# Kernel optimization log

Hardware: AMD Instinct MI355X
Metric: run time of the kernel (lower is better)

The kernel has to match this reference:

```python
import jax, jax.numpy as jnp
import numpy as np

N_USERS = 200000
N_ITEMS = 100000
N_NODES = N_USERS + N_ITEMS
N_EDGES = 1500000
EMBED_DIM = 64
BERT_DIM = 384
N_LAYERS = 3


def setup_inputs() -> dict:
    key = jax.random.key(0)
    ks = jax.random.split(key, 13)
    return {
        "user_emb": jax.random.normal(ks[0], (N_USERS, EMBED_DIM), jnp.float32) * 0.1,
        "item_emb": jax.random.normal(ks[1], (N_ITEMS, EMBED_DIM), jnp.float32) * 0.1,
        "gender_emb": jax.random.normal(ks[2], (3, EMBED_DIM), jnp.float32) * 0.1,
        "age_emb": jax.random.normal(ks[3], (8, EMBED_DIM), jnp.float32) * 0.1,
        "cat_emb": jax.random.normal(ks[4], (11, EMBED_DIM), jnp.float32) * 0.1,
        "bert_proj_w": jax.random.normal(ks[5], (EMBED_DIM, BERT_DIM), jnp.float32) * 0.05,
        "item_bert": jax.random.normal(ks[6], (N_ITEMS, BERT_DIM), jnp.float32),
        "adj_val": jax.random.uniform(ks[7], (N_EDGES,), jnp.float32),
        "user_gender": jax.random.randint(ks[8], (N_USERS,), 0, 3, jnp.int64 if jax.config.jax_enable_x64 else jnp.int32),
        "user_age": jax.random.randint(ks[9], (N_USERS,), 0, 8, jnp.int32),
        "item_cat": jax.random.randint(ks[10], (N_ITEMS,), 0, 11, jnp.int32),
        "adj_row": jax.random.randint(ks[11], (N_EDGES,), 0, N_NODES, jnp.int32),
        "adj_col": jax.random.randint(ks[12], (N_EDGES,), 0, N_NODES, jnp.int32),
    }


def reference(user_emb, item_emb, gender_emb, age_emb, cat_emb, bert_proj_w,
              item_bert, adj_val, user_gender, user_age, item_cat,
              adj_row, adj_col):
    n_users = user_emb.shape[0]
    n_nodes = n_users + item_emb.shape[0]

    # initial embeddings: base table + side-info gathers (+ projected BERT for items)
    u0 = user_emb + gender_emb[user_gender] + age_emb[user_age]          # [U, d]
    i0 = item_emb + cat_emb[item_cat] + item_bert @ bert_proj_w.T       # [I, d]
    all_emb = jnp.concatenate([u0, i0], axis=0)                          # [N, d]

    # COO SpMM: y[r] += val * x[c]
    def spmm(x):
        msgs = adj_val[:, None] * x[adj_col]                             # [E, d]
        return jax.ops.segment_sum(msgs, adj_row, num_segments=n_nodes)

    acc = all_emb
    x = all_emb
    for _ in range(N_LAYERS):
        x = spmm(x)
        acc = acc + x
    out = acc / (N_LAYERS + 1)                                           # mean over layer stack
    return out[:n_users], out[n_users:]
```

## Files before the change

kernel.cpp:

```cpp
#include <hip/hip_runtime.h>
#include <hip/hip_bf16.h>

#define NU 200000
#define NI 100000
#define NN 300000
#define NE 1500000
#define BD 384

#define SCAN1_BLOCKS 293
#define NBINS 293
#define CH 4096
#define P2CAP 6144

typedef __attribute__((ext_vector_type(8))) short short8;
typedef __attribute__((ext_vector_type(4))) float floatx4;

__device__ __forceinline__ void fma4(float4& a, float s, const float4& w) {
    a.x = fmaf(s, w.x, a.x);
    a.y = fmaf(s, w.y, a.y);
    a.z = fmaf(s, w.z, a.z);
    a.w = fmaf(s, w.w, a.w);
}

__device__ __forceinline__ float bf2f(unsigned short v) {
    union { unsigned int u; float f; } c; c.u = ((unsigned int)v) << 16; return c.f;
}
__device__ __forceinline__ float4 ub4f(const ushort4 v) {
    return make_float4(bf2f(v.x), bf2f(v.y), bf2f(v.z), bf2f(v.w));
}
__device__ __forceinline__ ushort4 f4bf(const float4 a) {
    union { __hip_bfloat16 b; unsigned short u; } c0, c1, c2, c3;
    c0.b = __float2bfloat16(a.x); c1.b = __float2bfloat16(a.y);
    c2.b = __float2bfloat16(a.z); c3.b = __float2bfloat16(a.w);
    return make_ushort4(c0.u, c1.u, c2.u, c3.u);
}

__device__ __forceinline__ short8 cvt8(const float4 a, const float4 b) {
    union { short8 v; __hip_bfloat16 e[8]; } u;
    u.e[0] = __float2bfloat16(a.x); u.e[1] = __float2bfloat16(a.y);
    u.e[2] = __float2bfloat16(a.z); u.e[3] = __float2bfloat16(a.w);
    u.e[4] = __float2bfloat16(b.x); u.e[5] = __float2bfloat16(b.y);
    u.e[6] = __float2bfloat16(b.z); u.e[7] = __float2bfloat16(b.w);
    return u.v;
}

__global__ __launch_bounds__(256) void user_init_k(
    const float4* __restrict__ user_emb,
    const float4* __restrict__ gender_emb,
    const float4* __restrict__ age_emb,
    const int* __restrict__ ug,
    const int* __restrict__ ua,
    float4* __restrict__ A)
{
    int i = blockIdx.x * 256 + threadIdx.x;
    int u = i >> 4, q = i & 15;
    float4 e = user_emb[i];
    float4 g = gender_emb[ug[u] * 16 + q];
    float4 a = age_emb[ua[u] * 16 + q];
    e.x += g.x + a.x; e.y += g.y + a.y; e.z += g.z + a.z; e.w += g.w + a.w;
    A[i] = e;
}

__global__ __launch_bounds__(256) void wconv_k(
    const float* __restrict__ W, short8* __restrict__ Wb)
{
    int t = blockIdx.x * 256 + threadIdx.x;
    if (t >= 3072) return;
    int lid = t & 63, nt = (t >> 6) & 3, kt = t >> 8;
    int m16 = lid & 15, q = lid >> 4;
    const float* src = W + (size_t)(nt * 16 + m16) * BD + kt * 32 + q * 8;
    Wb[t] = cvt8(*(const float4*)src, *(const float4*)(src + 4));
}

__global__ __launch_bounds__(256) void item_init_k(
    const float* __restrict__ bert,
    const short8* __restrict__ Wb,
    const float* __restrict__ item_emb,
    const float* __restrict__ cat_emb,
    const int* __restrict__ icat,
    float* __restrict__ A)
{
    const int lid = threadIdx.x & 63;
    const int wv  = threadIdx.x >> 6;
    const int i0  = (blockIdx.x * 4 + wv) * 16;
    if (i0 >= NI) return;
    const int m16 = lid & 15;
    const int q   = lid >> 4;

    const float*  ab = bert + (size_t)(i0 + m16) * BD + q * 8;
    const short8* wb = Wb + lid;

    floatx4 cf[4];
    cf[0] = (floatx4){0.f, 0.f, 0.f, 0.f};
    cf[1] = cf[0]; cf[2] = cf[0]; cf[3] = cf[0];

    float4 a0 = *(const float4*)(ab + 0);
    float4 a1 = *(const float4*)(ab + 4);
    short8 b0 = wb[0 * 64];
    short8 b1 = wb[1 * 64];
    short8 b2 = wb[2 * 64];
    short8 b3 = wb[3 * 64];

    #pragma unroll
    for (int kt = 0; kt < 11; ++kt) {
        float4 na0 = *(const float4*)(ab + (kt + 1) * 32 + 0);
        float4 na1 = *(const float4*)(ab + (kt + 1) * 32 + 4);
        short8 nb0 = wb[((kt + 1) * 4 + 0) * 64];
        short8 nb1 = wb[((kt + 1) * 4 + 1) * 64];
        short8 nb2 = wb[((kt + 1) * 4 + 2) * 64];
        short8 nb3 = wb[((kt + 1) * 4 + 3) * 64];
        short8 af = cvt8(a0, a1);
        cf[0] = __builtin_amdgcn_mfma_f32_16x16x32_bf16(af, b0, cf[0], 0, 0, 0);
        cf[1] = __builtin_amdgcn_mfma_f32_16x16x32_bf16(af, b1, cf[1], 0, 0, 0);
        cf[2] = __builtin_amdgcn_mfma_f32_16x16x32_bf16(af, b2, cf[2], 0, 0, 0);
        cf[3] = __builtin_amdgcn_mfma_f32_16x16x32_bf16(af, b3, cf[3], 0, 0, 0);
        a0 = na0; a1 = na1; b0 = nb0; b1 = nb1; b2 = nb2; b3 = nb3;
    }
    {
        short8 af = cvt8(a0, a1);
        cf[0] = __builtin_amdgcn_mfma_f32_16x16x32_bf16(af, b0, cf[0], 0, 0, 0);
        cf[1] = __builtin_amdgcn_mfma_f32_16x16x32_bf16(af, b1, cf[1], 0, 0, 0);
        cf[2] = __builtin_amdgcn_mfma_f32_16x16x32_bf16(af, b2, cf[2], 0, 0, 0);
        cf[3] = __builtin_amdgcn_mfma_f32_16x16x32_bf16(af, b3, cf[3], 0, 0, 0);
    }

    #pragma unroll
    for (int r = 0; r < 4; ++r) {
        const int item = i0 + q * 4 + r;
        const int cat  = icat[item];
        const size_t eb = (size_t)item * 64;
        const size_t abn = (size_t)(NU + item) * 64;
        #pragma unroll
        for (int td = 0; td < 4; ++td) {
            const int d = td * 16 + m16;
            A[abn + d] = cf[td][r] + item_emb[eb + d] + cat_emb[cat * 64 + d];
        }
    }
}

__global__ __launch_bounds__(256) void hist_k(
    const int* __restrict__ row, int* __restrict__ counts)
{
    int e = blockIdx.x * 256 + threadIdx.x;
    if (e < NE) atomicAdd(&counts[row[e]], 1);
}

__global__ __launch_bounds__(256) void scan1_k(
    const int* __restrict__ counts, int* __restrict__ offs,
    int* __restrict__ blksum)
{
    __shared__ int s[256];
    int t = threadIdx.x;
    int base = blockIdx.x * 1024 + t * 4;
    int c0 = 0, c1 = 0, c2 = 0, c3 = 0;
    if (base + 3 < NN) {
        int4 c = *(const int4*)&counts[base];
        c0 = c.x; c1 = c.y; c2 = c.z; c3 = c.w;
    } else {
        if (base + 0 < NN) c0 = counts[base + 0];
        if (base + 1 < NN) c1 = counts[base + 1];
        if (base + 2 < NN) c2 = counts[base + 2];
    }
    int tsum = c0 + c1 + c2 + c3;
    s[t] = tsum;
    __syncthreads();
    for (int d = 1; d < 256; d <<= 1) {
        int v = (t >= d) ? s[t - d] : 0;
        __syncthreads();
        s[t] += v;
        __syncthreads();
    }
    if (t == 255) blksum[blockIdx.x] = s[255];
    int e0 = s[t] - tsum, e1 = e0 + c0, e2 = e1 + c1, e3 = e2 + c2;
    if (base + 0 < NN) offs[base + 0] = e0;
    if (base + 1 < NN) offs[base + 1] = e1;
    if (base + 2 < NN) offs[base + 2] = e2;
    if (base + 3 < NN) offs[base + 3] = e3;
}

__global__ __launch_bounds__(512) void scan2_k(int* __restrict__ blksum)
{
    __shared__ int s[512];
    int t = threadIdx.x;
    int v = (t < SCAN1_BLOCKS) ? blksum[t] : 0;
    s[t] = v;
    __syncthreads();
    for (int d = 1; d < 512; d <<= 1) {
        int x = (t >= d) ? s[t - d] : 0;
        __syncthreads();
        s[t] += x;
        __syncthreads();
    }
    if (t < SCAN1_BLOCKS) blksum[t] = s[t] - v;
}

__global__ __launch_bounds__(256) void addoff_k(
    int* __restrict__ offs, const int* __restrict__ blkoff,
    int* __restrict__ cursor,
    int* __restrict__ binstart, int* __restrict__ bincur)
{
    int i = blockIdx.x * 256 + threadIdx.x;
    if (i < NN) {
        int o = offs[i] + blkoff[i >> 10];
        offs[i] = o;
        cursor[i] = o;
        if ((i & 1023) == 0) {
            binstart[i >> 10] = o;
            bincur[i >> 10] = o;
        }
    }
}

__global__ __launch_bounds__(256) void binscat_k(
    const int* __restrict__ row, const int* __restrict__ col,
    const float* __restrict__ val,
    int* __restrict__ bincur,
    int2* __restrict__ tcv, int* __restrict__ trow)
{
    __shared__ int lhist[512];
    __shared__ int lexcl[512];
    __shared__ int lbase[512];
    __shared__ int s[256];
    __shared__ int2 scv[CH];
    __shared__ int  srow[CH];

    int t = threadIdx.x;
    int e0 = blockIdx.x * CH;
    int n = NE - e0; if (n > CH) n = CH;

    lhist[t] = 0; lhist[t + 256] = 0;
    __syncthreads();

    int r[16]; int2 cv[16]; int rk[16];
    #pragma unroll
    for (int i = 0; i < 16; ++i) {
        int idx = e0 + i * 256 + t;
        if (idx < NE) {
            r[i] = row[idx];
            cv[i].x = col[idx];
            cv[i].y = __float_as_int(val[idx]);
            rk[i] = atomicAdd(&lhist[r[i] >> 10], 1);
        }
    }
    __syncthreads();

    int c0 = lhist[2 * t], c1 = lhist[2 * t + 1];
    int tsum = c0 + c1;
    s[t] = tsum;
    __syncthreads();
    for (int d = 1; d < 256; d <<= 1) {
        int v = (t >= d) ? s[t - d] : 0;
        __syncthreads();
        s[t] += v;
        __syncthreads();
    }
    int ex = s[t] - tsum;
    lexcl[2 * t] = ex; lexcl[2 * t + 1] = ex + c0;
    if (2 * t < NBINS && c0 > 0)     lbase[2 * t]     = atomicAdd(&bincur[2 * t], c0);
    if (2 * t + 1 < NBINS && c1 > 0) lbase[2 * t + 1] = atomicAdd(&bincur[2 * t + 1], c1);
    __syncthreads();

    #pragma unroll
    for (int i = 0; i < 16; ++i) {
        int idx = e0 + i * 256 + t;
        if (idx < NE) {
            int b = r[i] >> 10;
            int p = lexcl[b] + rk[i];
            scv[p] = cv[i];
            srow[p] = r[i];
        }
    }
    __syncthreads();

    for (int p = t; p < n; p += 256) {
        int rr = srow[p];
        int b = rr >> 10;
        int g = lbase[b] + (p - lexcl[b]);
        tcv[g] = scv[p];
        trow[g] = rr;
    }
}

__global__ __launch_bounds__(256) void scatter2_k(
    const int2* __restrict__ tcv, const int* __restrict__ trow,
    const int* __restrict__ binstart,
    int* __restrict__ cursor, int2* __restrict__ edges)
{
    __shared__ int2 scv[P2CAP];
    int b = blockIdx.x;
    int s = binstart[b];
    int e = (b + 1 < NBINS) ? binstart[b + 1] : NE;
    int cnt = e - s;

    if (cnt <= P2CAP) {
        for (int p = s + threadIdx.x; p < e; p += 256) {
            int rr = trow[p];
            int pos = atomicAdd(&cursor[rr], 1);
            scv[pos - s] = tcv[p];
        }
        __syncthreads();
        for (int p = threadIdx.x; p < cnt; p += 256)
            edges[s + p] = scv[p];
    } else {
        for (int p = s + threadIdx.x; p < e; p += 256) {
            int rr = trow[p];
            int pos = atomicAdd(&cursor[rr], 1);
            edges[pos] = tcv[p];
        }
    }
}

__global__ __launch_bounds__(256) void spmm_l1_k(
    const float4* __restrict__ x,
    ushort4* __restrict__ yb,
    float4* __restrict__ out,
    const int* __restrict__ offs,
    const int* __restrict__ ends,
    const int2* __restrict__ edges)
{
    int t = threadIdx.x;
    int r = blockIdx.x * 16 + (t >> 4);
    int q = t & 15;
    int s = offs[r], e = ends[r];
    float4 acc = make_float4(0.f, 0.f, 0.f, 0.f);
    int k = s;
    for (; k + 4 <= e; k += 4) {
        int2 c0 = edges[k + 0];
        int2 c1 = edges[k + 1];
        int2 c2 = edges[k + 2];
        int2 c3 = edges[k + 3];
        float4 x0 = x[c0.x * 16 + q];
        float4 x1 = x[c1.x * 16 + q];
        float4 x2 = x[c2.x * 16 + q];
        float4 x3 = x[c3.x * 16 + q];
        fma4(acc, __int_as_float(c0.y), x0);
        fma4(acc, __int_as_float(c1.y), x1);
        fma4(acc, __int_as_float(c2.y), x2);
        fma4(acc, __int_as_float(c3.y), x3);
    }
    for (; k < e; ++k) {
        int2 cv = edges[k];
        fma4(acc, __int_as_float(cv.y), x[cv.x * 16 + q]);
    }
    int oi = r * 16 + q;
    yb[oi] = f4bf(acc);
    float4 xr = x[oi];
    out[oi] = make_float4(0.25f * (xr.x + acc.x), 0.25f * (xr.y + acc.y),
                          0.25f * (xr.z + acc.z), 0.25f * (xr.w + acc.w));
}

__global__ __launch_bounds__(256) void spmm_bf_k(
    const ushort4* __restrict__ xb,
    ushort4* __restrict__ yb,
    float4* __restrict__ out,
    const int* __restrict__ offs,
    const int* __restrict__ ends,
    const int2* __restrict__ edges,
    int mode)
{
    int t = threadIdx.x;
    int r = blockIdx.x * 16 + (t >> 4);
    int q = t & 15;
    int s = offs[r], e = ends[r];
    float4 acc = make_float4(0.f, 0.f, 0.f, 0.f);
    int k = s;
    for (; k + 4 <= e; k += 4) {
        int2 c0 = edges[k + 0];
        int2 c1 = edges[k + 1];
        int2 c2 = edges[k + 2];
        int2 c3 = edges[k + 3];
        ushort4 v0 = xb[c0.x * 16 + q];
        ushort4 v1 = xb[c1.x * 16 + q];
        ushort4 v2 = xb[c2.x * 16 + q];
        ushort4 v3 = xb[c3.x * 16 + q];
        fma4(acc, __int_as_float(c0.y), ub4f(v0));
        fma4(acc, __int_as_float(c1.y), ub4f(v1));
        fma4(acc, __int_as_float(c2.y), ub4f(v2));
        fma4(acc, __int_as_float(c3.y), ub4f(v3));
    }
    for (; k < e; ++k) {
        int2 cv = edges[k];
        fma4(acc, __int_as_float(cv.y), ub4f(xb[cv.x * 16 + q]));
    }
    int oi = r * 16 + q;
    if (mode == 2) {
        yb[oi] = f4bf(acc);
    } else {
        float4 xr = ub4f(xb[oi]);
        float4 o = out[oi];
        o.x += 0.25f * (xr.x + acc.x);
        o.y += 0.25f * (xr.y + acc.y);
        o.z += 0.25f * (xr.z + acc.z);
        o.w += 0.25f * (xr.w + acc.w);
        out[oi] = o;
    }
}

extern "C" void kernel_launch(void* const* d_in, const int* in_sizes, int n_in,
                              void* d_out, int out_size, void* d_ws, size_t ws_size,
                              hipStream_t stream)
{
    const float* user_emb    = (const float*)d_in[0];
    const float* item_emb    = (const float*)d_in[1];
    const float* gender_emb  = (const float*)d_in[2];
    const float* age_emb     = (const float*)d_in[3];
    const float* cat_emb     = (const float*)d_in[4];
    const float* bert_w      = (const float*)d_in[5];
    const float* item_bert   = (const float*)d_in[6];
    const float* adj_val     = (const float*)d_in[7];
    const int*   user_gender = (const int*)d_in[8];
    const int*   user_age    = (const int*)d_in[9];
    const int*   item_cat    = (const int*)d_in[10];
    const int*   adj_row     = (const int*)d_in[11];
    const int*   adj_col     = (const int*)d_in[12];

    float* out = (float*)d_out;

    float* A       = (float*)d_ws;
    float* B       = A + (size_t)NN * 64;
    int2*  edges   = (int2*)(B + (size_t)NN * 64);
    int*   offs    = (int*)(edges + NE);
    int*   cursor  = offs + NN;
    int*   blksum  = cursor + NN;
    int*   binstart= blksum + 512;
    int*   bincur  = binstart + 512;
    short8* Wb     = (short8*)(bincur + 512);

    int2*    tcv  = (int2*)B;
    int*     trow = (int*)(tcv + NE);
    ushort4* B16  = (ushort4*)B;
    ushort4* A16  = B16 + (size_t)NN * 16;

    hipMemsetAsync(offs, 0, (size_t)NN * sizeof(int), stream);
    hist_k<<<5860, 256, 0, stream>>>(adj_row, offs);
    scan1_k<<<SCAN1_BLOCKS, 256, 0, stream>>>(offs, offs, blksum);
    scan2_k<<<1, 512, 0, stream>>>(blksum);
    addoff_k<<<1172, 256, 0, stream>>>(offs, blksum, cursor, binstart, bincur);
    binscat_k<<<367, 256, 0, stream>>>(adj_row, adj_col, adj_val, bincur, tcv, trow);
    scatter2_k<<<NBINS, 256, 0, stream>>>(tcv, trow, binstart, cursor, edges);

    wconv_k<<<12, 256, 0, stream>>>(bert_w, Wb);
    user_init_k<<<12500, 256, 0, stream>>>(
        (const float4*)user_emb, (const float4*)gender_emb, (const float4*)age_emb,
        user_gender, user_age, (float4*)A);
    item_init_k<<<1563, 256, 0, stream>>>(
        item_bert, Wb, item_emb, cat_emb, item_cat, A);

    spmm_l1_k<<<18750, 256, 0, stream>>>(
        (const float4*)A, B16, (float4*)out, offs, cursor, edges);
    spmm_bf_k<<<18750, 256, 0, stream>>>(
        B16, A16, (float4*)out, offs, cursor, edges, 2);
    spmm_bf_k<<<18750, 256, 0, stream>>>(
        A16, B16, (float4*)out, offs, cursor, edges, 3);
}
```

Measured before the change: 651.6 us.

## Store initial embeddings in bf16 and fuse layer-mean output into final SpMM

The user and item init kernels now write the layer-0 embeddings as bf16, so the first SpMM gathers half the bytes. The separate fp32 first-layer kernel and the read-modify-write of the output are removed. The final layer kernel sums bf16 copies of layers 0–2 with its own accumulator and writes the mean once. This trades extra bf16 rounding of the initial embeddings for lower gather and output traffic.

```diff
diff --git a/kernel.cpp b/kernel.cpp
--- a/kernel.cpp
+++ b/kernel.cpp
@@ -28,11 +28,11 @@
 __device__ __forceinline__ float4 ub4f(const ushort4 v) {
     return make_float4(bf2f(v.x), bf2f(v.y), bf2f(v.z), bf2f(v.w));
 }
+__device__ __forceinline__ unsigned short f2bfu(float x) {
+    union { __hip_bfloat16 b; unsigned short u; } c; c.b = __float2bfloat16(x); return c.u;
+}
 __device__ __forceinline__ ushort4 f4bf(const float4 a) {
-    union { __hip_bfloat16 b; unsigned short u; } c0, c1, c2, c3;
-    c0.b = __float2bfloat16(a.x); c1.b = __float2bfloat16(a.y);
-    c2.b = __float2bfloat16(a.z); c3.b = __float2bfloat16(a.w);
-    return make_ushort4(c0.u, c1.u, c2.u, c3.u);
+    return make_ushort4(f2bfu(a.x), f2bfu(a.y), f2bfu(a.z), f2bfu(a.w));
 }
 
 __device__ __forceinline__ short8 cvt8(const float4 a, const float4 b) {
@@ -50,7 +50,7 @@
     const float4* __restrict__ age_emb,
     const int* __restrict__ ug,
     const int* __restrict__ ua,
-    float4* __restrict__ A)
+    ushort4* __restrict__ A0)
 {
     int i = blockIdx.x * 256 + threadIdx.x;
     int u = i >> 4, q = i & 15;
@@ -58,7 +58,7 @@
     float4 g = gender_emb[ug[u] * 16 + q];
     float4 a = age_emb[ua[u] * 16 + q];
     e.x += g.x + a.x; e.y += g.y + a.y; e.z += g.z + a.z; e.w += g.w + a.w;
-    A[i] = e;
+    A0[i] = f4bf(e);
 }
 
 __global__ __launch_bounds__(256) void wconv_k(
@@ -78,7 +78,7 @@
     const float* __restrict__ item_emb,
     const float* __restrict__ cat_emb,
     const int* __restrict__ icat,
-    float* __restrict__ A)
+    unsigned short* __restrict__ A0)
 {
     const int lid = threadIdx.x & 63;
     const int wv  = threadIdx.x >> 6;
@@ -133,7 +133,7 @@
         #pragma unroll
         for (int td = 0; td < 4; ++td) {
             const int d = td * 16 + m16;
-            A[abn + d] = cf[td][r] + item_emb[eb + d] + cat_emb[cat * 64 + d];
+            A0[abn + d] = f2bfu(cf[td][r] + item_emb[eb + d] + cat_emb[cat * 64 + d]);
         }
     }
 }
@@ -310,53 +310,12 @@
     }
 }
 
-__global__ __launch_bounds__(256) void spmm_l1_k(
-    const float4* __restrict__ x,
+__global__ __launch_bounds__(256) void spmm_bf_k(
+    const ushort4* __restrict__ xb,
     ushort4* __restrict__ yb,
-    float4* __restrict__ out,
     const int* __restrict__ offs,
     const int* __restrict__ ends,
     const int2* __restrict__ edges)
-{
-    int t = threadIdx.x;
-    int r = blockIdx.x * 16 + (t >> 4);
-    int q = t & 15;
-    int s = offs[r], e = ends[r];
-    float4 acc = make_float4(0.f, 0.f, 0.f, 0.f);
-    int k = s;
-    for (; k + 4 <= e; k += 4) {
-        int2 c0 = edges[k + 0];
-        int2 c1 = edges[k + 1];
-        int2 c2 = edges[k + 2];
-        int2 c3 = edges[k + 3];
-        float4 x0 = x[c0.x * 16 + q];
-        float4 x1 = x[c1.x * 16 + q];
-        float4 x2 = x[c2.x * 16 + q];
-        float4 x3 = x[c3.x * 16 + q];
-        fma4(acc, __int_as_float(c0.y), x0);
-        fma4(acc, __int_as_float(c1.y), x1);
-        fma4(acc, __int_as_float(c2.y), x2);
-        fma4(acc, __int_as_float(c3.y), x3);
-    }
-    for (; k < e; ++k) {
-        int2 cv = edges[k];
-        fma4(acc, __int_as_float(cv.y), x[cv.x * 16 + q]);
-    }
-    int oi = r * 16 + q;
-    yb[oi] = f4bf(acc);
-    float4 xr = x[oi];
-    out[oi] = make_float4(0.25f * (xr.x + acc.x), 0.25f * (xr.y + acc.y),
-                          0.25f * (xr.z + acc.z), 0.25f * (xr.w + acc.w));
-}
-
-__global__ __launch_bounds__(256) void spmm_bf_k(
-    const ushort4* __restrict__ xb,
-    ushort4* __restrict__ yb,
-    float4* __restrict__ out,
-    const int* __restrict__ offs,
-    const int* __restrict__ ends,
-    const int2* __restrict__ edges,
-    int mode)
 {
     int t = threadIdx.x;
     int r = blockIdx.x * 16 + (t >> 4);
@@ -382,18 +341,50 @@
         int2 cv = edges[k];
         fma4(acc, __int_as_float(cv.y), ub4f(xb[cv.x * 16 + q]));
     }
+    yb[r * 16 + q] = f4bf(acc);
+}
+
+__global__ __launch_bounds__(256) void spmm_l3_k(
+    const ushort4* __restrict__ xb,
+    const ushort4* __restrict__ x0b,
+    const ushort4* __restrict__ x1b,
+    float4* __restrict__ out,
+    const int* __restrict__ offs,
+    const int* __restrict__ ends,
+    const int2* __restrict__ edges)
+{
+    int t = threadIdx.x;
+    int r = blockIdx.x * 16 + (t >> 4);
+    int q = t & 15;
+    int s = offs[r], e = ends[r];
+    float4 acc = make_float4(0.f, 0.f, 0.f, 0.f);
+    int k = s;
+    for (; k + 4 <= e; k += 4) {
+        int2 c0 = edges[k + 0];
+        int2 c1 = edges[k + 1];
+        int2 c2 = edges[k + 2];
+        int2 c3 = edges[k + 3];
+        ushort4 v0 = xb[c0.x * 16 + q];
+        ushort4 v1 = xb[c1.x * 16 + q];
+        ushort4 v2 = xb[c2.x * 16 + q];
+        ushort4 v3 = xb[c3.x * 16 + q];
+        fma4(acc, __int_as_float(c0.y), ub4f(v0));
+        fma4(acc, __int_as_float(c1.y), ub4f(v1));
+        fma4(acc, __int_as_float(c2.y), ub4f(v2));
+        fma4(acc, __int_as_float(c3.y), ub4f(v3));
+    }
+    for (; k < e; ++k) {
+        int2 cv = edges[k];
+        fma4(acc, __int_as_float(cv.y), ub4f(xb[cv.x * 16 + q]));
+    }
     int oi = r * 16 + q;
-    if (mode == 2) {
-        yb[oi] = f4bf(acc);
-    } else {
-        float4 xr = ub4f(xb[oi]);
-        float4 o = out[oi];
-        o.x += 0.25f * (xr.x + acc.x);
-        o.y += 0.25f * (xr.y + acc.y);
-        o.z += 0.25f * (xr.z + acc.z);
-        o.w += 0.25f * (xr.w + acc.w);
-        out[oi] = o;
-    }
+    float4 x0 = ub4f(x0b[oi]);
+    float4 x1 = ub4f(x1b[oi]);
+    float4 x2 = ub4f(xb[oi]);
+    out[oi] = make_float4(0.25f * (x0.x + x1.x + x2.x + acc.x),
+                          0.25f * (x0.y + x1.y + x2.y + acc.y),
+                          0.25f * (x0.z + x1.z + x2.z + acc.z),
+                          0.25f * (x0.w + x1.w + x2.w + acc.w));
 }
 
 extern "C" void kernel_launch(void* const* d_in, const int* in_sizes, int n_in,
@@ -426,6 +417,7 @@
     int*   bincur  = binstart + 512;
     short8* Wb     = (short8*)(bincur + 512);
 
+    ushort4* A0_16 = (ushort4*)A;
     int2*    tcv  = (int2*)B;
     int*     trow = (int*)(tcv + NE);
     ushort4* B16  = (ushort4*)B;
@@ -442,14 +434,12 @@
     wconv_k<<<12, 256, 0, stream>>>(bert_w, Wb);
     user_init_k<<<12500, 256, 0, stream>>>(
         (const float4*)user_emb, (const float4*)gender_emb, (const float4*)age_emb,
-        user_gender, user_age, (float4*)A);
+        user_gender, user_age, A0_16);
     item_init_k<<<1563, 256, 0, stream>>>(
-        item_bert, Wb, item_emb, cat_emb, item_cat, A);
-
-    spmm_l1_k<<<18750, 256, 0, stream>>>(
-        (const float4*)A, B16, (float4*)out, offs, cursor, edges);
-    spmm_bf_k<<<18750, 256, 0, stream>>>(
-        B16, A16, (float4*)out, offs, cursor, edges, 2);
-    spmm_bf_k<<<18750, 256, 0, stream>>>(
-        A16, B16, (float4*)out, offs, cursor, edges, 3);
-}
+        item_bert, Wb, item_emb, cat_emb, item_cat, (unsigned short*)A0_16);
+
+    spmm_bf_k<<<18750, 256, 0, stream>>>(A0_16, B16, offs, cursor, edges);
+    spmm_bf_k<<<18750, 256, 0, stream>>>(B16, A16, offs, cursor, edges);
+    spmm_l3_k<<<18750, 256, 0, stream>>>(A16, A0_16, B16, (float4*)out,
+                                         offs, cursor, edges);
+}
```

After: 624.2 us. 4.2% less time.
